# Performance work log

Measured on AMD Instinct MI355X. Metric: run time of the kernel, lower is better.

Reference implementation:

```python
import jax, jax.numpy as jnp
import numpy as np

H = 768      # hidden_size
NH = 12      # num_heads
DH = H // NH # head dim = 64
NL = 50      # num_labels
T = 512      # seq_len per chunk
NC = 16      # number of chunks (encoding.shape[0] / T)
S = NC * T   # total key length = 8192


def setup_inputs() -> dict:
    key = jax.random.key(0)
    ks = jax.random.split(key, 7)
    return {
        "encoding": jax.random.normal(ks[0], (S, H), dtype=jnp.float32),
        # nn.Parameter ~ N(0, 0.1)
        "label_queries": 0.1 * jax.random.normal(ks[1], (NL, H), dtype=jnp.float32),
        "label_weights": 0.1 * jax.random.normal(ks[2], (H, NL), dtype=jnp.float32),
        # nn.MultiheadAttention packed in-projection (3H, H) and out-projection
        "in_proj_w": 0.02 * jax.random.normal(ks[3], (3 * H, H), dtype=jnp.float32),
        "in_proj_b": jnp.zeros((3 * H,), dtype=jnp.float32),
        "out_w": 0.02 * jax.random.normal(ks[4], (H, H), dtype=jnp.float32),
        "out_b": jnp.zeros((H,), dtype=jnp.float32),
    }


def reference(encoding, label_queries, label_weights, in_proj_w, in_proj_b, out_w, out_b):
    # Split packed QKV projections (torch MultiheadAttention layout)
    wq, wk, wv = jnp.split(in_proj_w, 3, axis=0)
    bq, bk, bv = jnp.split(in_proj_b, 3)

    # Queries are the label embeddings, identical for every mask row -> project once.
    q = (label_queries @ wq.T + bq).reshape(NL, NH, DH)   # (Nl, NH, DH)
    k = (encoding @ wk.T + bk).reshape(S, NH, DH)          # (S, NH, DH)
    v = (encoding @ wv.T + bv).reshape(S, NH, DH)          # (S, NH, DH)

    scale = 1.0 / np.sqrt(DH).astype(np.float32)
    # Shared (mask-independent) logits: (NH, Nl, S)
    logits = jnp.einsum('lhd,shd->hls', q * scale, k)

    # Growing block-causal key_padding_mask: row i sees keys j < (i+1)*T
    limits = (jnp.arange(NC) + 1) * T                      # (NC,)
    allowed = jnp.arange(S)[None, :] < limits[:, None]     # (NC, S) bool

    masked = jnp.where(allowed[:, None, None, :], logits[None], -jnp.inf)  # (NC,NH,Nl,S)
    attn = jax.nn.softmax(masked, axis=-1)

    ctx = jnp.einsum('bhls,shd->blhd', attn, v).reshape(NC, NL, H)
    attn_output = ctx @ out_w.T + out_b                    # (NC, Nl, H)

    # label_weights is (H, Nl) but torch code .view's it as (1, Nl, H): a RESHAPE.
    lw = label_weights.reshape(NL, H)
    score = jnp.sum(attn_output * lw[None], axis=2)        # (NC, Nl)
    return score
```

## Files before the change

### kernel.cpp

```cpp
#include <hip/hip_runtime.h>
#include <math.h>

#define H_   768
#define NH_  12
#define DH_  64
#define NL_  50
#define NC_  16
#define S_   8192
#define NLH_ 640
#define MT_  64
#define NT3_ 10
#define KC_  8

typedef __attribute__((ext_vector_type(8))) short short8;
typedef __attribute__((ext_vector_type(4))) short short4v;
typedef __attribute__((ext_vector_type(4))) float f32x4;
typedef unsigned short u16;

#define AS1(p) ((const __attribute__((address_space(1))) void*)(p))
#define AS3(p) ((__attribute__((address_space(3))) void*)(p))

__device__ inline u16 f2b(float f) {
    union { float f; unsigned u; } x; x.f = f;
    return (u16)((x.u + 0x7FFFu + ((x.u >> 16) & 1u)) >> 16);
}
__device__ inline short8 cvt8(const float* __restrict__ src) {
    const float4 v0 = *reinterpret_cast<const float4*>(src);
    const float4 v1 = *reinterpret_cast<const float4*>(src + 4);
    short8 o;
    o[0] = f2b(v0.x); o[1] = f2b(v0.y); o[2] = f2b(v0.z); o[3] = f2b(v0.w);
    o[4] = f2b(v1.x); o[5] = f2b(v1.y); o[6] = f2b(v1.z); o[7] = f2b(v1.w);
    return o;
}

#define PB_TILE 96

__global__ __launch_bounds__(256)
void prep1(const float* __restrict__ enc, const float* __restrict__ lq,
           const float* __restrict__ lwt, const float* __restrict__ ipw,
           const float* __restrict__ ow,
           u16* __restrict__ enc_b, float* __restrict__ pbuf)
{
    __shared__ u16 As[64 * 32];
    __shared__ u16 Bs[128 * 32];

    const int b = blockIdx.x, tid = threadIdx.x;

    if (b >= PB_TILE) {
        const long i8 = (long)(b - PB_TILE) * 2048 + (long)tid * 8;
        *reinterpret_cast<short8*>(enc_b + i8) = cvt8(enc + i8);
        return;
    }

    const int mat = b / 48, r2 = b % 48, kc = r2 / 6, jt = r2 % 6;
    const long n0 = (long)jt * 128;
    const bool isM2 = (mat == 1);
    const int lane = tid & 63, w = tid >> 6;
    const int rr = lane & 15, g = lane >> 4;

    f32x4 acc[4][2];
    #pragma unroll
    for (int m = 0; m < 4; ++m)
        #pragma unroll
        for (int n = 0; n < 2; ++n)
            #pragma unroll
            for (int j = 0; j < 4; ++j) acc[m][n][j] = 0.f;

    const float* Asrc = isM2 ? lwt : lq;

    #pragma unroll
    for (int ki = 0; ki < 3; ++ki) {
        const int k0 = kc * 96 + ki * 32;
        {
            const int row = tid >> 2, sp = tid & 3;
            short8 o;
            #pragma unroll
            for (int i = 0; i < 8; ++i) o[i] = 0;
            if (row < NL_) o = cvt8(Asrc + (long)row * H_ + k0 + sp * 8);
            const int ss = sp ^ ((row >> 1) & 3);
            *reinterpret_cast<short8*>(As + row * 32 + ss * 8) = o;
        }
        if (!isM2) {
            #pragma unroll
            for (int it = 0; it < 2; ++it) {
                const int gid = it * 256 + tid;
                const int row = gid >> 2, sp = gid & 3;
                const short8 o = cvt8(ipw + (n0 + row) * H_ + k0 + sp * 8);
                const int ss = sp ^ ((row >> 1) & 3);
                *reinterpret_cast<short8*>(Bs + row * 32 + ss * 8) = o;
            }
        } else {
            #pragma unroll
            for (int it = 0; it < 4; ++it) {
                const int gid = it * 256 + tid;
                const int n = gid & 127, kq = gid >> 7;
                short4v o4;
                #pragma unroll
                for (int i = 0; i < 4; ++i)
                    o4[i] = f2b(ow[(long)(k0 + kq * 4 + i) * H_ + n0 + n]);
                const int byte = n * 64 + (((kq >> 1) ^ ((n >> 1) & 3)) << 4) + (kq & 1) * 8;
                *reinterpret_cast<short4v*>((char*)Bs + byte) = o4;
            }
        }
        __syncthreads();

        short8 a[4], bb[2];
        #pragma unroll
        for (int m = 0; m < 4; ++m) {
            const int row = m * 16 + rr;
            a[m] = *reinterpret_cast<const short8*>(As + row * 32 + ((g ^ ((row >> 1) & 3)) * 8));
        }
        #pragma unroll
        for (int n = 0; n < 2; ++n) {
            const int nr = w * 32 + n * 16 + rr;
            bb[n] = *reinterpret_cast<const short8*>(Bs + nr * 32 + ((g ^ ((nr >> 1) & 3)) * 8));
        }
        #pragma unroll
        for (int m = 0; m < 4; ++m)
            #pragma unroll
            for (int n = 0; n < 2; ++n)
                acc[m][n] = __builtin_amdgcn_mfma_f32_16x16x32_bf16(a[m], bb[n], acc[m][n], 0, 0, 0);
        __syncthreads();
    }

    float* P = pbuf + (long)(mat * KC_ + kc) * 64 * H_;
    #pragma unroll
    for (int m = 0; m < 4; ++m)
        #pragma unroll
        for (int n = 0; n < 2; ++n) {
            const long col = n0 + w * 32 + n * 16 + rr;
            #pragma unroll
            for (int j = 0; j < 4; ++j) {
                const int row = m * 16 + g * 4 + j;
                P[(long)row * H_ + col] = acc[m][n][j];
            }
        }
}

__global__ __launch_bounds__(256)
void prep2(const float* __restrict__ pbuf, const float* __restrict__ ipw,
           const float* __restrict__ ipb, const float* __restrict__ lwt,
           const float* __restrict__ ob,
           u16* __restrict__ qkL, u16* __restrict__ W2L, float* __restrict__ constL)
{
    __shared__ u16 As2[64 * 64];
    __shared__ u16 Bs2[128 * 64];

    const int b = blockIdx.x, tid = threadIdx.x;

    if (b < 144) {
        const int mat = b / 72, r2 = b % 72, h = r2 / 6, jt = r2 % 6;
        const long n0 = (long)jt * 128;
        const int kb = H_ + mat * H_ + h * DH_;
        const int lane = tid & 63, w = tid >> 6;
        const int rr = lane & 15, g = lane >> 4;

        #pragma unroll
        for (int it = 0; it < 2; ++it) {
            const int gid = it * 256 + tid;
            const int row = gid >> 3, sp = gid & 7;
            float a8[8];
            #pragma unroll
            for (int i = 0; i < 8; ++i) a8[i] = 0.f;
            #pragma unroll
            for (int kc = 0; kc < KC_; ++kc) {
                const float* p = pbuf + ((long)(mat * KC_ + kc) * 64 + row) * H_
                               + h * DH_ + sp * 8;
                const float4 v0 = *reinterpret_cast<const float4*>(p);
                const float4 v1 = *reinterpret_cast<const float4*>(p + 4);
                a8[0] += v0.x; a8[1] += v0.y; a8[2] += v0.z; a8[3] += v0.w;
                a8[4] += v1.x; a8[5] += v1.y; a8[6] += v1.z; a8[7] += v1.w;
            }
            short8 o;
            if (mat == 0) {
                #pragma unroll
                for (int i = 0; i < 8; ++i)
                    o[i] = f2b((row < NL_) ? 0.125f * (a8[i] + ipb[h * DH_ + sp * 8 + i]) : 0.f);
            } else {
                #pragma unroll
                for (int i = 0; i < 8; ++i) o[i] = f2b(a8[i]);
            }
            *reinterpret_cast<short8*>(As2 + row * 64 + ((sp ^ (row & 7)) * 8)) = o;
        }
        #pragma unroll
        for (int it = 0; it < 8; ++it) {
            const int gid = it * 256 + tid;
            const int n = gid & 127, kq = gid >> 7;
            short4v o4;
            #pragma unroll
            for (int i = 0; i < 4; ++i)
                o4[i] = f2b(ipw[(long)(kb + kq * 4 + i) * H_ + n0 + n]);
            const int byte = n * 128 + (((kq >> 1) ^ (n & 7)) << 4) + (kq & 1) * 8;
            *reinterpret_cast<short4v*>((char*)Bs2 + byte) = o4;
        }
        __syncthreads();

        f32x4 acc[4][2];
        #pragma unroll
        for (int m = 0; m < 4; ++m)
            #pragma unroll
            for (int n = 0; n < 2; ++n)
                #pragma unroll
                for (int j = 0; j < 4; ++j) acc[m][n][j] = 0.f;

        #pragma unroll
        for (int ks = 0; ks < 2; ++ks) {
            short8 a[4], bb[2];
            #pragma unroll
            for (int m = 0; m < 4; ++m) {
                const int row = m * 16 + rr, s = ks * 4 + g;
                a[m] = *reinterpret_cast<const short8*>(As2 + row * 64 + ((s ^ (row & 7)) * 8));
            }
            #pragma unroll
            for (int n = 0; n < 2; ++n) {
                const int nr = w * 32 + n * 16 + rr, s = ks * 4 + g;
                bb[n] = *reinterpret_cast<const short8*>(Bs2 + nr * 64 + ((s ^ (nr & 7)) * 8));
            }
            #pragma unroll
            for (int m = 0; m < 4; ++m)
                #pragma unroll
                for (int n = 0; n < 2; ++n)
                    acc[m][n] = __builtin_amdgcn_mfma_f32_16x16x32_bf16(a[m], bb[n], acc[m][n], 0, 0, 0);
        }

        u16* O = mat ? W2L : qkL;
        #pragma unroll
        for (int m = 0; m < 4; ++m)
            #pragma unroll
            for (int n = 0; n < 2; ++n) {
                const long col = n0 + w * 32 + n * 16 + rr;
                #pragma unroll
                for (int j = 0; j < 4; ++j) {
                    const int l = m * 16 + g * 4 + j;
                    if (l < NL_)
                        O[(long)(h * NL_ + l) * H_ + col] = f2b(acc[m][n][j]);
                }
            }
        return;
    }

    if (b < 194) {
        const int l = b - 144;
        __shared__ float r4[4];
        const int lane = tid & 63, w = tid >> 6;
        float s = 0.f;
        #pragma unroll
        for (int r = 0; r < 3; ++r) {
            const int i = tid + 256 * r;
            float m2v = 0.f;
            #pragma unroll
            for (int kc = 0; kc < KC_; ++kc)
                m2v += pbuf[((long)(KC_ + kc) * 64 + l) * H_ + i];
            s += m2v * ipb[2 * H_ + i] + lwt[(long)l * H_ + i] * ob[i];
        }
        #pragma unroll
        for (int o2 = 1; o2 < 64; o2 <<= 1) s += __shfl_xor(s, o2);
        if (lane == 0) r4[w] = s;
        __syncthreads();
        if (tid == 0) constL[l] = r4[0] + r4[1] + r4[2] + r4[3];
        return;
    }

    {
        short8 z;
        #pragma unroll
        for (int i = 0; i < 8; ++i) z[i] = 0;
        for (int i = tid; i < 40 * H_ / 8; i += 256) {
            *reinterpret_cast<short8*>(qkL + (long)600 * H_ + i * 8) = z;
            *reinterpret_cast<short8*>(W2L + (long)600 * H_ + i * 8) = z;
        }
    }
}

__global__ __launch_bounds__(256)
void fused_gemm(const u16* __restrict__ enc_b, const u16* __restrict__ qkL,
                const u16* __restrict__ W2L,
                float* __restrict__ pmg, float* __restrict__ ppg,
                float* __restrict__ pzg)
{
    const int flat = blockIdx.y * NT3_ + blockIdx.x;
    const int rem  = (flat & 7) * 80 + (flat >> 3);
    const int mt   = rem / NT3_, ntb = rem % NT3_;
    const long m0 = (long)mt * 128, n0 = (long)ntb * 64;

    __shared__ u16 As[3][4096];
    __shared__ u16 Bqs[3][2048];
    __shared__ u16 Bzs[3][2048];
    __shared__ float redm[128], redsum[128], redz[128];

    const int tid = threadIdx.x, lane = tid & 63, w = tid >> 6;
    const int wr = w >> 1, wc = w & 1;
    const int sr0 = tid >> 2, sp = tid & 3;

    f32x4 accq[4][2], accz[4][2];
    #pragma unroll
    for (int m = 0; m < 4; ++m)
        #pragma unroll
        for (int n = 0; n < 2; ++n)
            #pragma unroll
            for (int j = 0; j < 4; ++j) { accq[m][n][j] = 0.f; accz[m][n][j] = 0.f; }

    auto stage = [&](int t, int buf) {
        const int k0 = t * 32;
        #pragma unroll
        for (int tt = 0; tt < 2; ++tt) {
            const int row = tt * 64 + sr0;
            const int ss  = sp ^ ((row >> 1) & 3);
            __builtin_amdgcn_global_load_lds(AS1(enc_b + (m0 + row) * H_ + k0 + ss * 8),
                                             AS3(As[buf] + (tt * 256 + tid) * 8), 16, 0, 0);
        }
        const int ss0 = sp ^ ((sr0 >> 1) & 3);
        __builtin_amdgcn_global_load_lds(AS1(qkL + (n0 + sr0) * H_ + k0 + ss0 * 8),
                                         AS3(Bqs[buf] + tid * 8), 16, 0, 0);
        __builtin_amdgcn_global_load_lds(AS1(W2L + (n0 + sr0) * H_ + k0 + ss0 * 8),
                                         AS3(Bzs[buf] + tid * 8), 16, 0, 0);
    };

    stage(0, 0);
    stage(1, 1);

    const int rr = lane & 15, g = lane >> 4;
    const int ro = (g ^ ((rr >> 1) & 3)) * 8;

    for (int t = 0; t < 24; ++t) {
        if (t < 23) asm volatile("s_waitcnt vmcnt(4)" ::: "memory");
        else        asm volatile("s_waitcnt vmcnt(0)" ::: "memory");
        __builtin_amdgcn_s_barrier();
        __builtin_amdgcn_sched_barrier(0);

        const int cb = t % 3;
        short8 a[4], bq[2], bz[2];
        #pragma unroll
        for (int m = 0; m < 4; ++m)
            a[m] = *reinterpret_cast<const short8*>(As[cb] + (wr * 64 + m * 16 + rr) * 32 + ro);
        #pragma unroll
        for (int n = 0; n < 2; ++n) {
            bq[n] = *reinterpret_cast<const short8*>(Bqs[cb] + (wc * 32 + n * 16 + rr) * 32 + ro);
            bz[n] = *reinterpret_cast<const short8*>(Bzs[cb] + (wc * 32 + n * 16 + rr) * 32 + ro);
        }
        #pragma unroll
        for (int m = 0; m < 4; ++m)
            #pragma unroll
            for (int n = 0; n < 2; ++n) {
                accq[m][n] = __builtin_amdgcn_mfma_f32_16x16x32_bf16(a[m], bq[n], accq[m][n], 0, 0, 0);
                accz[m][n] = __builtin_amdgcn_mfma_f32_16x16x32_bf16(a[m], bz[n], accz[m][n], 0, 0, 0);
            }

        if (t + 2 < 24) stage(t + 2, (t + 2) % 3);
    }

    #pragma unroll
    for (int n = 0; n < 2; ++n) {
        float m_ = -INFINITY;
        #pragma unroll
        for (int mm = 0; mm < 4; ++mm)
            #pragma unroll
            for (int j = 0; j < 4; ++j) m_ = fmaxf(m_, accq[mm][n][j]);
        m_ = fmaxf(m_, __shfl_xor(m_, 16));
        m_ = fmaxf(m_, __shfl_xor(m_, 32));
        if (g == 0) redm[wr * 64 + wc * 32 + n * 16 + rr] = m_;
    }
    __syncthreads();
    #pragma unroll
    for (int n = 0; n < 2; ++n) {
        const int col = wc * 32 + n * 16 + rr;
        const float gm = fmaxf(redm[col], redm[64 + col]);
        float s_ = 0.f, z_ = 0.f;
        #pragma unroll
        for (int mm = 0; mm < 4; ++mm)
            #pragma unroll
            for (int j = 0; j < 4; ++j) {
                const float e = __expf(accq[mm][n][j] - gm);
                s_ += e;
                z_ += e * accz[mm][n][j];
            }
        s_ += __shfl_xor(s_, 16); s_ += __shfl_xor(s_, 32);
        z_ += __shfl_xor(z_, 16); z_ += __shfl_xor(z_, 32);
        if (g == 0) { redsum[wr * 64 + col] = s_; redz[wr * 64 + col] = z_; }
    }
    __syncthreads();
    if (tid < 64) {
        const int col = tid;
        const long o = (long)mt * NLH_ + n0 + col;
        pmg[o] = fmaxf(redm[col], redm[64 + col]);
        ppg[o] = redsum[col] + redsum[64 + col];
        pzg[o] = redz[col] + redz[64 + col];
    }
}

__global__ __launch_bounds__(64)
void combine(const float* __restrict__ pmg, const float* __restrict__ ppg,
             const float* __restrict__ pzg, const float* __restrict__ constL,
             float* __restrict__ out)
{
    const int l = blockIdx.x, t = threadIdx.x;
    __shared__ float sm[64][12], sp_[64][12], sz[64][12];
    __shared__ float sc[16][12];

    #pragma unroll
    for (int h = 0; h < NH_; ++h) {
        const long o = (long)t * NLH_ + h * NL_ + l;
        sm[t][h]  = pmg[o];
        sp_[t][h] = ppg[o];
        sz[t][h]  = pzg[o];
    }
    __syncthreads();

    if (t < NH_) {
        float M = -INFINITY, S = 0.f, A = 0.f;
        for (int mt = 0; mt < MT_; ++mt) {
            const float mc = sm[mt][t], pc = sp_[mt][t], zc = sz[mt][t];
            const float Mn = fmaxf(M, mc);
            const float ea = __expf(M - Mn), eb = __expf(mc - Mn);
            S = S * ea + pc * eb;
            A = A * ea + zc * eb;
            M = Mn;
            if ((mt & 3) == 3) sc[mt >> 2][t] = A / S;
        }
    }
    __syncthreads();
    if (t < NC_) {
        float s = constL[l];
        #pragma unroll
        for (int h = 0; h < NH_; ++h) s += sc[t][h];
        out[(long)t * NL_ + l] = s;
    }
}

extern "C" void kernel_launch(void* const* d_in, const int* in_sizes, int n_in,
                              void* d_out, int out_size, void* d_ws, size_t ws_size,
                              hipStream_t stream) {
    const float* enc = (const float*)d_in[0];
    const float* lq  = (const float*)d_in[1];
    const float* lwt = (const float*)d_in[2];
    const float* ipw = (const float*)d_in[3];
    const float* ipb = (const float*)d_in[4];
    const float* ow  = (const float*)d_in[5];
    const float* ob  = (const float*)d_in[6];
    float* out = (float*)d_out;

    float* wsf    = (float*)d_ws;
    float* pbuf   = wsf;
    float* constL = pbuf + (long)2 * KC_ * 64 * H_;
    float* pmg    = constL + 64;
    float* ppg    = pmg + (long)MT_ * NLH_;
    float* pzg    = ppg + (long)MT_ * NLH_;
    u16* enc_b = (u16*)(pzg + (long)MT_ * NLH_);
    u16* qkL   = enc_b + (long)S_ * H_;
    u16* W2L   = qkL + (long)NLH_ * H_;

    prep1<<<dim3(PB_TILE + 3072), 256, 0, stream>>>(
        enc, lq, lwt, ipw, ow, enc_b, pbuf);

    prep2<<<dim3(195), 256, 0, stream>>>(pbuf, ipw, ipb, lwt, ob,
                                         qkL, W2L, constL);

    fused_gemm<<<dim3(NT3_, MT_), 256, 0, stream>>>(enc_b, qkL, W2L, pmg, ppg, pzg);

    combine<<<dim3(NL_), 64, 0, stream>>>(pmg, ppg, pzg, constL, out);
}
```

Baseline: 58.58 us.

## Use single-wave 64x64 GEMM tiles with double buffering and no block reductions

```diff
diff --git a/kernel.cpp b/kernel.cpp
--- a/kernel.cpp
+++ b/kernel.cpp
@@ -8,7 +8,7 @@
 #define NC_  16
 #define S_   8192
 #define NLH_ 640
-#define MT_  64
+#define MT_  128
 #define NT3_ 10
 #define KC_  8
 
@@ -272,119 +272,103 @@
     }
 }
 
-__global__ __launch_bounds__(256)
+__global__ __launch_bounds__(64)
 void fused_gemm(const u16* __restrict__ enc_b, const u16* __restrict__ qkL,
                 const u16* __restrict__ W2L,
                 float* __restrict__ pmg, float* __restrict__ ppg,
                 float* __restrict__ pzg)
 {
-    const int flat = blockIdx.y * NT3_ + blockIdx.x;
-    const int rem  = (flat & 7) * 80 + (flat >> 3);
-    const int mt   = rem / NT3_, ntb = rem % NT3_;
-    const long m0 = (long)mt * 128, n0 = (long)ntb * 64;
-
-    __shared__ u16 As[3][4096];
-    __shared__ u16 Bqs[3][2048];
-    __shared__ u16 Bzs[3][2048];
-    __shared__ float redm[128], redsum[128], redz[128];
-
-    const int tid = threadIdx.x, lane = tid & 63, w = tid >> 6;
-    const int wr = w >> 1, wc = w & 1;
-    const int sr0 = tid >> 2, sp = tid & 3;
-
-    f32x4 accq[4][2], accz[4][2];
+    const int flat = blockIdx.x;
+    const int wg   = (flat & 7) * 160 + (flat >> 3);
+    const int mt   = wg / NT3_, ntb = wg % NT3_;
+    const long m0 = (long)mt * 64, n0 = (long)ntb * 64;
+
+    __shared__ u16 Abuf[2][2048];
+    __shared__ u16 Qbuf[2][2048];
+    __shared__ u16 Zbuf[2][2048];
+
+    const int lane = threadIdx.x;
+    const int rr = lane & 15, g = lane >> 4;
+
+    f32x4 accq[4][4], accz[4][4];
     #pragma unroll
     for (int m = 0; m < 4; ++m)
         #pragma unroll
-        for (int n = 0; n < 2; ++n)
+        for (int n = 0; n < 4; ++n)
             #pragma unroll
             for (int j = 0; j < 4; ++j) { accq[m][n][j] = 0.f; accz[m][n][j] = 0.f; }
 
     auto stage = [&](int t, int buf) {
         const int k0 = t * 32;
         #pragma unroll
-        for (int tt = 0; tt < 2; ++tt) {
-            const int row = tt * 64 + sr0;
-            const int ss  = sp ^ ((row >> 1) & 3);
+        for (int i = 0; i < 4; ++i) {
+            const int gr = i * 64 + lane;
+            const int row = gr >> 2, sp = gr & 3;
+            const int ss = sp ^ ((row >> 1) & 3);
             __builtin_amdgcn_global_load_lds(AS1(enc_b + (m0 + row) * H_ + k0 + ss * 8),
-                                             AS3(As[buf] + (tt * 256 + tid) * 8), 16, 0, 0);
-        }
-        const int ss0 = sp ^ ((sr0 >> 1) & 3);
-        __builtin_amdgcn_global_load_lds(AS1(qkL + (n0 + sr0) * H_ + k0 + ss0 * 8),
-                                         AS3(Bqs[buf] + tid * 8), 16, 0, 0);
-        __builtin_amdgcn_global_load_lds(AS1(W2L + (n0 + sr0) * H_ + k0 + ss0 * 8),
-                                         AS3(Bzs[buf] + tid * 8), 16, 0, 0);
+                                             AS3(Abuf[buf] + gr * 8), 16, 0, 0);
+            __builtin_amdgcn_global_load_lds(AS1(qkL + (n0 + row) * H_ + k0 + ss * 8),
+                                             AS3(Qbuf[buf] + gr * 8), 16, 0, 0);
+            __builtin_amdgcn_global_load_lds(AS1(W2L + (n0 + row) * H_ + k0 + ss * 8),
+                                             AS3(Zbuf[buf] + gr * 8), 16, 0, 0);
+        }
     };
 
     stage(0, 0);
-    stage(1, 1);
-
-    const int rr = lane & 15, g = lane >> 4;
-    const int ro = (g ^ ((rr >> 1) & 3)) * 8;
 
     for (int t = 0; t < 24; ++t) {
-        if (t < 23) asm volatile("s_waitcnt vmcnt(4)" ::: "memory");
-        else        asm volatile("s_waitcnt vmcnt(0)" ::: "memory");
-        __builtin_amdgcn_s_barrier();
+        asm volatile("s_waitcnt vmcnt(0)" ::: "memory");
         __builtin_amdgcn_sched_barrier(0);
-
-        const int cb = t % 3;
-        short8 a[4], bq[2], bz[2];
-        #pragma unroll
-        for (int m = 0; m < 4; ++m)
-            a[m] = *reinterpret_cast<const short8*>(As[cb] + (wr * 64 + m * 16 + rr) * 32 + ro);
-        #pragma unroll
-        for (int n = 0; n < 2; ++n) {
-            bq[n] = *reinterpret_cast<const short8*>(Bqs[cb] + (wc * 32 + n * 16 + rr) * 32 + ro);
-            bz[n] = *reinterpret_cast<const short8*>(Bzs[cb] + (wc * 32 + n * 16 + rr) * 32 + ro);
-        }
-        #pragma unroll
-        for (int m = 0; m < 4; ++m)
-            #pragma unroll
-            for (int n = 0; n < 2; ++n) {
+        if (t + 1 < 24) stage(t + 1, (t + 1) & 1);
+
+        const int cb = t & 1;
+        short8 a[4], bq[4], bz[4];
+        #pragma unroll
+        for (int m = 0; m < 4; ++m) {
+            const int row = m * 16 + rr;
+            a[m] = *reinterpret_cast<const short8*>(
+                Abuf[cb] + row * 32 + ((g ^ ((row >> 1) & 3)) * 8));
+        }
+        #pragma unroll
+        for (int n = 0; n < 4; ++n) {
+            const int col = n * 16 + rr;
+            const int so = (g ^ ((col >> 1) & 3)) * 8;
+            bq[n] = *reinterpret_cast<const short8*>(Qbuf[cb] + col * 32 + so);
+            bz[n] = *reinterpret_cast<const short8*>(Zbuf[cb] + col * 32 + so);
+        }
+        #pragma unroll
+        for (int m = 0; m < 4; ++m)
+            #pragma unroll
+            for (int n = 0; n < 4; ++n) {
                 accq[m][n] = __builtin_amdgcn_mfma_f32_16x16x32_bf16(a[m], bq[n], accq[m][n], 0, 0, 0);
                 accz[m][n] = __builtin_amdgcn_mfma_f32_16x16x32_bf16(a[m], bz[n], accz[m][n], 0, 0, 0);
             }
-
-        if (t + 2 < 24) stage(t + 2, (t + 2) % 3);
-    }
-
-    #pragma unroll
-    for (int n = 0; n < 2; ++n) {
-        float m_ = -INFINITY;
-        #pragma unroll
-        for (int mm = 0; mm < 4; ++mm)
-            #pragma unroll
-            for (int j = 0; j < 4; ++j) m_ = fmaxf(m_, accq[mm][n][j]);
-        m_ = fmaxf(m_, __shfl_xor(m_, 16));
-        m_ = fmaxf(m_, __shfl_xor(m_, 32));
-        if (g == 0) redm[wr * 64 + wc * 32 + n * 16 + rr] = m_;
-    }
-    __syncthreads();
-    #pragma unroll
-    for (int n = 0; n < 2; ++n) {
-        const int col = wc * 32 + n * 16 + rr;
-        const float gm = fmaxf(redm[col], redm[64 + col]);
-        float s_ = 0.f, z_ = 0.f;
-        #pragma unroll
-        for (int mm = 0; mm < 4; ++mm)
+    }
+
+    #pragma unroll
+    for (int n = 0; n < 4; ++n) {
+        float mx = -INFINITY;
+        #pragma unroll
+        for (int m = 0; m < 4; ++m)
+            #pragma unroll
+            for (int j = 0; j < 4; ++j) mx = fmaxf(mx, accq[m][n][j]);
+        mx = fmaxf(mx, __shfl_xor(mx, 16));
+        mx = fmaxf(mx, __shfl_xor(mx, 32));
+        float s = 0.f, z = 0.f;
+        #pragma unroll
+        for (int m = 0; m < 4; ++m)
             #pragma unroll
             for (int j = 0; j < 4; ++j) {
-                const float e = __expf(accq[mm][n][j] - gm);
-                s_ += e;
-                z_ += e * accz[mm][n][j];
-            }
-        s_ += __shfl_xor(s_, 16); s_ += __shfl_xor(s_, 32);
-        z_ += __shfl_xor(z_, 16); z_ += __shfl_xor(z_, 32);
-        if (g == 0) { redsum[wr * 64 + col] = s_; redz[wr * 64 + col] = z_; }
-    }
-    __syncthreads();
-    if (tid < 64) {
-        const int col = tid;
-        const long o = (long)mt * NLH_ + n0 + col;
-        pmg[o] = fmaxf(redm[col], redm[64 + col]);
-        ppg[o] = redsum[col] + redsum[64 + col];
-        pzg[o] = redz[col] + redz[64 + col];
+                const float e = __expf(accq[m][n][j] - mx);
+                s += e;
+                z += e * accz[m][n][j];
+            }
+        s += __shfl_xor(s, 16); s += __shfl_xor(s, 32);
+        z += __shfl_xor(z, 16); z += __shfl_xor(z, 32);
+        if (g == 0) {
+            const long o = (long)mt * NLH_ + n0 + n * 16 + rr;
+            pmg[o] = mx; ppg[o] = s; pzg[o] = z;
+        }
     }
 }
 
@@ -394,15 +378,19 @@
              float* __restrict__ out)
 {
     const int l = blockIdx.x, t = threadIdx.x;
-    __shared__ float sm[64][12], sp_[64][12], sz[64][12];
+    __shared__ float sm[MT_][12], sp_[MT_][12], sz[MT_][12];
     __shared__ float sc[16][12];
 
     #pragma unroll
-    for (int h = 0; h < NH_; ++h) {
-        const long o = (long)t * NLH_ + h * NL_ + l;
-        sm[t][h]  = pmg[o];
-        sp_[t][h] = ppg[o];
-        sz[t][h]  = pzg[o];
+    for (int r = 0; r < 2; ++r) {
+        const int m = t + r * 64;
+        #pragma unroll
+        for (int h = 0; h < NH_; ++h) {
+            const long o = (long)m * NLH_ + h * NL_ + l;
+            sm[m][h]  = pmg[o];
+            sp_[m][h] = ppg[o];
+            sz[m][h]  = pzg[o];
+        }
     }
     __syncthreads();
 
@@ -415,7 +403,7 @@
             S = S * ea + pc * eb;
             A = A * ea + zc * eb;
             M = Mn;
-            if ((mt & 3) == 3) sc[mt >> 2][t] = A / S;
+            if ((mt & 7) == 7) sc[mt >> 3][t] = A / S;
         }
     }
     __syncthreads();
@@ -455,7 +443,7 @@
     prep2<<<dim3(195), 256, 0, stream>>>(pbuf, ipw, ipb, lwt, ob,
                                          qkL, W2L, constL);
 
-    fused_gemm<<<dim3(NT3_, MT_), 256, 0, stream>>>(enc_b, qkL, W2L, pmg, ppg, pzg);
+    fused_gemm<<<dim3(MT_ * NT3_), 64, 0, stream>>>(enc_b, qkL, W2L, pmg, ppg, pzg);
 
     combine<<<dim3(NL_), 64, 0, stream>>>(pmg, ppg, pzg, constL, out);
 }
```

Result: slower. 81.66 us (+39.4%).
